# Optimization experiments

Measured on AMD Instinct MI355X. Metric: run time of the kernel, lower is better.

## Reference

```python
import jax, jax.numpy as jnp
import numpy as np

B, S, D = 8, 2048, 768

def setup_inputs():
    key = jax.random.key(0)
    k1, k2, k3, k4 = jax.random.split(key, 4)
    hidden = jax.random.normal(k1, (B, S, D), dtype=jnp.float32)
    # relative lengths in [0.5, 1.0) so every sequence has a realistic valid region
    lengths = 0.5 + 0.5 * jax.random.uniform(k2, (B,), dtype=jnp.float32)
    s = 1.0 / np.sqrt(D)
    W1 = jax.random.uniform(k3, (D, D), minval=-s, maxval=s, dtype=jnp.float32)
    b1 = jnp.zeros((D,), jnp.float32)
    W2 = jax.random.uniform(k4, (D,), minval=-s, maxval=s, dtype=jnp.float32)
    b2 = jnp.zeros((), jnp.float32)
    return {"hidden": hidden, "lengths": lengths, "W1": W1, "b1": b1, "W2": W2, "b2": b2}

def _boundaries(hidden, lengths, W1, b1, W2, b2):
    # Eval-mode boundary prediction (dropout = identity, soft = probs).
    Bn, Sn, _ = hidden.shape
    actual_lens = (lengths * Sn).astype(jnp.int32)                      # [B]
    valid = (jnp.arange(Sn)[None, :] < actual_lens[:, None]).astype(hidden.dtype)  # [B,S]
    h = jax.nn.gelu(hidden @ W1 + b1, approximate=False)                # torch nn.GELU is exact
    logits = h @ W2 + b2                                                # [B,S]
    probs = jax.nn.sigmoid(logits)
    soft = probs * valid
    hard = (probs > 0.5).astype(hidden.dtype) * valid
    last_valid = jnp.clip(actual_lens - 1, 0, Sn - 1)
    bi = jnp.arange(Bn)
    soft = soft.at[bi, last_valid].set(1.0)
    hard = hard.at[bi, last_valid].set(1.0)
    hard_b = hard - jax.lax.stop_gradient(soft) + soft                  # straight-through
    return hard_b, probs * valid, valid, actual_lens

def reference(hidden, lengths, W1, b1, W2, b2):
    Bn, Sn, Dn = hidden.shape
    hard_b, masked_probs, valid, actual_lens = _boundaries(hidden, lengths, W1, b1, W2, b2)
    # K = max segments in the batch (data-dependent -> computed eagerly, as
    # the original torch code does with .item() inside common()).
    K = int(jnp.max(jnp.sum(jax.lax.stop_gradient(hard_b), axis=1)))
    # segment id of each position: boundary token ENDS its segment
    seg_id = jnp.cumsum(hard_b, axis=1) - hard_b                        # [B,S]
    seg_onehot = (jnp.arange(K)[None, None, :]
                  == jax.lax.stop_gradient(seg_id)[:, :, None])          # [B,S,K] == (foo==0)
    segment_mask = seg_onehot.astype(hidden.dtype) * valid[:, :, None]
    counts = jnp.maximum(segment_mask.sum(axis=1), 1.0)                 # [B,K]
    # dense one-hot mask-matmul segment mean, matching the torch bmm formulation
    pooled = jnp.einsum('bsk,bsd->bkd', segment_mask, hidden) / counts[:, :, None]
    nb = (hard_b * valid).sum(axis=1)                                   # boundaries / sample
    max_segments = max(K, 1)
    full = nb >= max_segments - 1
    partial = (nb > 0) & (nb < max_segments - 1)
    shortened = jnp.where(full, 1.0,
                          jnp.where(partial, (nb + 1.0) / max_segments, 0.0))
    return pooled, masked_probs, shortened, nb, actual_lens.astype(jnp.float32)
```

## Files before the change

### kernel.cpp

```cpp
#include <hip/hip_runtime.h>
#include <math.h>

typedef __bf16 bf16x8 __attribute__((ext_vector_type(8)));
typedef float  f32x4  __attribute__((ext_vector_type(4)));

#define NT2 12

__device__ inline float gelu_f(float x) {
    return 0.5f * x * (1.0f + erff(x * 0.70710678118654752f));
}

typedef const __attribute__((address_space(1))) void* gas_t;
typedef __attribute__((address_space(3))) void*       las_t;
__device__ __forceinline__ void gl_lds16(const void* g, void* l) {
    __builtin_amdgcn_global_load_lds((gas_t)g, (las_t)l, 16, 0, 0);
}

__global__ __launch_bounds__(256) void s0_w1t(
    const float* __restrict__ W1, __bf16* __restrict__ Wt, int Dn)
{
    __shared__ float tile[32][33];
    const int k0 = blockIdx.x * 32;
    const int n0 = blockIdx.y * 32;
    const int tx = threadIdx.x & 31, ty = threadIdx.x >> 5;
    #pragma unroll
    for (int p = 0; p < 4; ++p)
        tile[ty + p * 8][tx] = W1[(size_t)(k0 + ty + p * 8) * Dn + n0 + tx];
    __syncthreads();
    #pragma unroll
    for (int p = 0; p < 4; ++p) {
        const int n = n0 + ty + p * 8, k = k0 + tx;
        Wt[(size_t)n * Dn + k] = (__bf16)tile[tx][ty + p * 8];
    }
}

__global__ __launch_bounds__(512) void k1_f32(
    const float* __restrict__ X, const __bf16* __restrict__ W1t,
    const float* __restrict__ b1, const float* __restrict__ W2,
    float* __restrict__ partial, int Kd)
{
    __shared__ float  Asf[2][128 * 32];
    __shared__ __bf16 Bsh[2][128 * 32];

    const int t    = threadIdx.x;
    const int lane = t & 63;
    const int w    = t >> 6;
    const int wr   = w >> 1;
    const int wc   = w & 1;
    const int ln15 = lane & 15, lg = lane >> 4;
    const int m0   = blockIdx.x * 128;
    const int n0   = blockIdx.y * 128;

    const int ar0 = t >> 3, alc = t & 7;
    const int ar1 = ar0 + 64;
    const float* gA0 = X + (size_t)(m0 + ar0) * Kd + (alc ^ (ar0 & 7)) * 4;
    const float* gA1 = X + (size_t)(m0 + ar1) * Kd + (alc ^ (ar1 & 7)) * 4;

    const int brow = t >> 2;
    const int bkw  = (t & 3) ^ ((brow >> 1) & 3);
    const __bf16* gB = W1t + (size_t)(n0 + brow) * Kd + bkw * 8;

    int aoff0[2], aoff1[2], boff[4];
    #pragma unroll
    for (int mf = 0; mf < 2; ++mf) {
        const int r = wr * 32 + mf * 16 + ln15;
        aoff0[mf] = r * 32 + ((2 * lg)     ^ (r & 7)) * 4;
        aoff1[mf] = r * 32 + ((2 * lg + 1) ^ (r & 7)) * 4;
    }
    #pragma unroll
    for (int nf = 0; nf < 4; ++nf) {
        const int r = wc * 64 + nf * 16 + ln15;
        boff[nf] = r * 32 + (lg ^ ((r >> 1) & 3)) * 8;
    }

    f32x4 acc[2][4];
    #pragma unroll
    for (int i = 0; i < 2; ++i)
        #pragma unroll
        for (int j = 0; j < 4; ++j)
            acc[i][j] = (f32x4){0.f, 0.f, 0.f, 0.f};

    gl_lds16(gA0, &Asf[0][t * 4]);
    gl_lds16(gA1, &Asf[0][(t + 512) * 4]);
    gl_lds16(gB,  &Bsh[0][t * 8]);
    __syncthreads();

    const int nt = Kd / 32;
    int cur = 0;
    for (int kt = 0; kt < nt; ++kt) {
        if (kt + 1 < nt) {
            const int ko = (kt + 1) * 32;
            gl_lds16(gA0 + ko, &Asf[cur ^ 1][t * 4]);
            gl_lds16(gA1 + ko, &Asf[cur ^ 1][(t + 512) * 4]);
            gl_lds16(gB  + ko, &Bsh[cur ^ 1][t * 8]);
        }
        bf16x8 fa[2], fb[4];
        #pragma unroll
        for (int mf = 0; mf < 2; ++mf) {
            const f32x4 lo = *(const f32x4*)&Asf[cur][aoff0[mf]];
            const f32x4 hi = *(const f32x4*)&Asf[cur][aoff1[mf]];
            #pragma unroll
            for (int i = 0; i < 4; ++i) {
                fa[mf][i]     = (__bf16)lo[i];
                fa[mf][4 + i] = (__bf16)hi[i];
            }
        }
        #pragma unroll
        for (int nf = 0; nf < 4; ++nf)
            fb[nf] = *(const bf16x8*)&Bsh[cur][boff[nf]];
        #pragma unroll
        for (int mf = 0; mf < 2; ++mf)
            #pragma unroll
            for (int nf = 0; nf < 4; ++nf)
                acc[mf][nf] = __builtin_amdgcn_mfma_f32_16x16x32_bf16(
                    fa[mf], fb[nf], acc[mf][nf], 0, 0, 0);
        __syncthreads();
        cur ^= 1;
    }

    float b1v[4], w2v[4];
    #pragma unroll
    for (int nf = 0; nf < 4; ++nf) {
        const int n = n0 + wc * 64 + nf * 16 + ln15;
        b1v[nf] = b1[n];
        w2v[nf] = W2[n];
    }
    #pragma unroll
    for (int mf = 0; mf < 2; ++mf)
        #pragma unroll
        for (int j = 0; j < 4; ++j) {
            float s = 0.f;
            #pragma unroll
            for (int nf = 0; nf < 4; ++nf) {
                float c = acc[mf][nf][j] + b1v[nf];
                s += gelu_f(c) * w2v[nf];
            }
            s += __shfl_xor(s, 1);
            s += __shfl_xor(s, 2);
            s += __shfl_xor(s, 4);
            s += __shfl_xor(s, 8);
            if (ln15 == 0) {
                const int m = m0 + wr * 32 + mf * 16 + lg * 4 + j;
                partial[(size_t)m * NT2 + blockIdx.y * 2 + wc] = s;
            }
        }
}

__global__ __launch_bounds__(256) void k2a_logits(
    const float* __restrict__ partial, const float* __restrict__ lengths,
    const float* __restrict__ b2p, float* __restrict__ logits,
    float* __restrict__ out_probs, int S)
{
    const int idx = blockIdx.x * 256 + threadIdx.x;
    const int b = idx / S, s = idx - b * S;
    float sum = b2p[0];
    #pragma unroll
    for (int jt = 0; jt < NT2; ++jt)
        sum += partial[(size_t)idx * NT2 + jt];
    logits[idx] = sum;
    const int len = (int)(lengths[b] * (float)S);
    out_probs[idx] = (s < len) ? 1.0f / (1.0f + expf(-sum)) : 0.0f;
}

__global__ __launch_bounds__(256) void k2b_scan(
    const float* __restrict__ logits, const float* __restrict__ lengths,
    float* __restrict__ out_short, float* __restrict__ out_nb,
    float* __restrict__ out_lens, int* __restrict__ bpos,
    int* __restrict__ nb_arr, int S, int K)
{
    const int b = blockIdx.x;
    const int t = threadIdx.x;
    const int len = (int)(lengths[b] * (float)S);

    __shared__ int cnt[256];
    __shared__ int flags_s[2048];

    const int RP = S / 256;
    const int base_s = t * RP;
    int local = 0;
    #pragma unroll
    for (int r = 0; r < 8; ++r) {
        int s = base_s + r;
        bool v = (s < len);
        int f = (s == len - 1) ? 1 : ((v && logits[(size_t)b * S + s] > 0.0f) ? 1 : 0);
        flags_s[s] = f;
        local += f;
    }
    cnt[t] = local;
    __syncthreads();
    for (int off = 1; off < 256; off <<= 1) {
        int v = cnt[t];
        int u = (t >= off) ? cnt[t - off] : 0;
        __syncthreads();
        cnt[t] = v + u;
        __syncthreads();
    }
    int excl = cnt[t] - local;
    int total = cnt[255];
    for (int r = 0; r < RP; ++r) {
        int s = base_s + r;
        if (flags_s[s]) { bpos[b * S + excl] = s; ++excl; }
    }
    if (t == 0) {
        nb_arr[b] = total;
        float nbf = (float)total;
        float Kf  = (float)K;
        out_nb[b]   = nbf;
        out_lens[b] = (float)len;
        float sh;
        if (nbf >= Kf - 1.0f)      sh = 1.0f;
        else if (nbf > 0.0f)       sh = (nbf + 1.0f) / Kf;
        else                       sh = 0.0f;
        out_short[b] = sh;
    }
}

__global__ __launch_bounds__(192) void k3_pool(
    const float* __restrict__ X, const int* __restrict__ bpos,
    const int* __restrict__ nb_arr, float* __restrict__ pooled,
    int S, int D, int K)
{
    const int bk = blockIdx.x;
    const int b  = bk / K;
    const int k  = bk - b * K;
    const int t  = threadIdx.x;
    const int nb = nb_arr[b];

    float4 acc = {0.f, 0.f, 0.f, 0.f};
    if (k < nb) {
        int start = (k == 0) ? 0 : (bpos[b * S + k - 1] + 1);
        int end   = bpos[b * S + k] + 1;
        float cntf = (float)(end - start);
        for (int s = start; s < end; ++s) {
            const float4 v = *(const float4*)&X[((size_t)b * S + s) * D + t * 4];
            acc.x += v.x; acc.y += v.y; acc.z += v.z; acc.w += v.w;
        }
        acc.x /= cntf; acc.y /= cntf; acc.z /= cntf; acc.w /= cntf;
    }
    *(float4*)&pooled[((size_t)b * K + k) * D + t * 4] = acc;
}

extern "C" void kernel_launch(void* const* d_in, const int* in_sizes, int n_in,
                              void* d_out, int out_size, void* d_ws, size_t ws_size,
                              hipStream_t stream) {
    const float* hidden  = (const float*)d_in[0];
    const float* lengths = (const float*)d_in[1];
    const float* W1      = (const float*)d_in[2];
    const float* b1      = (const float*)d_in[3];
    const float* W2      = (const float*)d_in[4];
    const float* b2      = (const float*)d_in[5];

    const int B = in_sizes[1];
    const int D = in_sizes[3];
    const int S = in_sizes[0] / (B * D);
    const int M = B * S;
    const int K = (out_size - B * S - 3 * B) / (B * D);

    float* out_pooled = (float*)d_out;
    float* out_probs  = out_pooled + (size_t)B * K * D;
    float* out_short  = out_probs + (size_t)B * S;
    float* out_nb     = out_short + B;
    float* out_lens   = out_nb + B;

    char* wsp = (char*)d_ws;
    float* partial = (float*)wsp; wsp += (size_t)M * NT2 * sizeof(float);
    float* logits  = (float*)wsp; wsp += (size_t)M * sizeof(float);
    int*   bpos    = (int*)wsp;   wsp += (size_t)M * sizeof(int);
    int*   nb_arr  = (int*)wsp;

    __bf16* W1t = (__bf16*)out_pooled;

    dim3 gs(D / 32, D / 32);
    s0_w1t<<<gs, 256, 0, stream>>>(W1, W1t, D);

    dim3 g1(M / 128, D / 128);
    k1_f32<<<g1, 512, 0, stream>>>(hidden, W1t, b1, W2, partial, D);

    k2a_logits<<<M / 256, 256, 0, stream>>>(partial, lengths, b2, logits,
                                            out_probs, S);
    k2b_scan<<<B, 256, 0, stream>>>(logits, lengths, out_short, out_nb,
                                    out_lens, bpos, nb_arr, S, K);
    k3_pool<<<B * K, D / 4, 0, stream>>>(hidden, bpos, nb_arr, out_pooled, S, D, K);
}
```

Measured before the change: 59.29 us.

## Pre-convert hidden to bf16, triple-buffer GEMM loads, pool from bf16 copy

Adds a pass that converts hidden to a bf16 workspace copy. The GEMM now streams bf16 A tiles through a three-stage LDS ring with explicit vmcnt waits and one barrier per k-step, instead of loading fp32 tiles and converting them in the inner loop. The segment pooling also reads the bf16 copy, which halves its read traffic but lowers the precision of the pooled means compared with the fp32 reference. The extra conversion pass adds a full read of hidden plus a bf16 write.

```diff
diff --git a/kernel.cpp b/kernel.cpp
--- a/kernel.cpp
+++ b/kernel.cpp
@@ -34,13 +34,29 @@
     }
 }
 
-__global__ __launch_bounds__(512) void k1_f32(
-    const float* __restrict__ X, const __bf16* __restrict__ W1t,
+__global__ __launch_bounds__(256) void s0_xb(
+    const float* __restrict__ X, __bf16* __restrict__ Xb, int n8)
+{
+    const int i = blockIdx.x * 256 + threadIdx.x;
+    if (i < n8) {
+        const float4 v0 = *(const float4*)(X + (size_t)i * 8);
+        const float4 v1 = *(const float4*)(X + (size_t)i * 8 + 4);
+        bf16x8 o;
+        o[0] = (__bf16)v0.x; o[1] = (__bf16)v0.y;
+        o[2] = (__bf16)v0.z; o[3] = (__bf16)v0.w;
+        o[4] = (__bf16)v1.x; o[5] = (__bf16)v1.y;
+        o[6] = (__bf16)v1.z; o[7] = (__bf16)v1.w;
+        *(bf16x8*)(Xb + (size_t)i * 8) = o;
+    }
+}
+
+__global__ __launch_bounds__(512) void k1_p3(
+    const __bf16* __restrict__ Xb, const __bf16* __restrict__ W1t,
     const float* __restrict__ b1, const float* __restrict__ W2,
     float* __restrict__ partial, int Kd)
 {
-    __shared__ float  Asf[2][128 * 32];
-    __shared__ __bf16 Bsh[2][128 * 32];
+    __shared__ __bf16 Ash[3][128 * 32];
+    __shared__ __bf16 Bsh[3][128 * 32];
 
     const int t    = threadIdx.x;
     const int lane = t & 63;
@@ -51,21 +67,16 @@
     const int m0   = blockIdx.x * 128;
     const int n0   = blockIdx.y * 128;
 
-    const int ar0 = t >> 3, alc = t & 7;
-    const int ar1 = ar0 + 64;
-    const float* gA0 = X + (size_t)(m0 + ar0) * Kd + (alc ^ (ar0 & 7)) * 4;
-    const float* gA1 = X + (size_t)(m0 + ar1) * Kd + (alc ^ (ar1 & 7)) * 4;
-
-    const int brow = t >> 2;
-    const int bkw  = (t & 3) ^ ((brow >> 1) & 3);
-    const __bf16* gB = W1t + (size_t)(n0 + brow) * Kd + bkw * 8;
-
-    int aoff0[2], aoff1[2], boff[4];
+    const int srow = t >> 2;
+    const int sgkw = (t & 3) ^ ((srow >> 1) & 3);
+    const __bf16* gA = Xb  + (size_t)(m0 + srow) * Kd + sgkw * 8;
+    const __bf16* gB = W1t + (size_t)(n0 + srow) * Kd + sgkw * 8;
+
+    int aoff[2], boff[4];
     #pragma unroll
     for (int mf = 0; mf < 2; ++mf) {
         const int r = wr * 32 + mf * 16 + ln15;
-        aoff0[mf] = r * 32 + ((2 * lg)     ^ (r & 7)) * 4;
-        aoff1[mf] = r * 32 + ((2 * lg + 1) ^ (r & 7)) * 4;
+        aoff[mf] = r * 32 + (lg ^ ((r >> 1) & 3)) * 8;
     }
     #pragma unroll
     for (int nf = 0; nf < 4; ++nf) {
@@ -80,43 +91,39 @@
         for (int j = 0; j < 4; ++j)
             acc[i][j] = (f32x4){0.f, 0.f, 0.f, 0.f};
 
-    gl_lds16(gA0, &Asf[0][t * 4]);
-    gl_lds16(gA1, &Asf[0][(t + 512) * 4]);
-    gl_lds16(gB,  &Bsh[0][t * 8]);
-    __syncthreads();
+    gl_lds16(gA,      &Ash[0][t * 8]);
+    gl_lds16(gB,      &Bsh[0][t * 8]);
+    gl_lds16(gA + 32, &Ash[1][t * 8]);
+    gl_lds16(gB + 32, &Bsh[1][t * 8]);
 
     const int nt = Kd / 32;
-    int cur = 0;
     for (int kt = 0; kt < nt; ++kt) {
-        if (kt + 1 < nt) {
-            const int ko = (kt + 1) * 32;
-            gl_lds16(gA0 + ko, &Asf[cur ^ 1][t * 4]);
-            gl_lds16(gA1 + ko, &Asf[cur ^ 1][(t + 512) * 4]);
-            gl_lds16(gB  + ko, &Bsh[cur ^ 1][t * 8]);
-        }
+        asm volatile("s_waitcnt vmcnt(2)" ::: "memory");
+        __builtin_amdgcn_s_barrier();
+        __builtin_amdgcn_sched_barrier(0);
+
+        const int cb = kt % 3;
         bf16x8 fa[2], fb[4];
         #pragma unroll
-        for (int mf = 0; mf < 2; ++mf) {
-            const f32x4 lo = *(const f32x4*)&Asf[cur][aoff0[mf]];
-            const f32x4 hi = *(const f32x4*)&Asf[cur][aoff1[mf]];
-            #pragma unroll
-            for (int i = 0; i < 4; ++i) {
-                fa[mf][i]     = (__bf16)lo[i];
-                fa[mf][4 + i] = (__bf16)hi[i];
-            }
-        }
+        for (int mf = 0; mf < 2; ++mf)
+            fa[mf] = *(const bf16x8*)&Ash[cb][aoff[mf]];
         #pragma unroll
         for (int nf = 0; nf < 4; ++nf)
-            fb[nf] = *(const bf16x8*)&Bsh[cur][boff[nf]];
+            fb[nf] = *(const bf16x8*)&Bsh[cb][boff[nf]];
         #pragma unroll
         for (int mf = 0; mf < 2; ++mf)
             #pragma unroll
             for (int nf = 0; nf < 4; ++nf)
                 acc[mf][nf] = __builtin_amdgcn_mfma_f32_16x16x32_bf16(
                     fa[mf], fb[nf], acc[mf][nf], 0, 0, 0);
-        __syncthreads();
-        cur ^= 1;
-    }
+
+        const int kn = (kt + 2 < nt) ? (kt + 2) : (nt - 1);
+        const int ko = kn * 32;
+        const int nb = (kt + 2) % 3;
+        gl_lds16(gA + ko, &Ash[nb][t * 8]);
+        gl_lds16(gB + ko, &Bsh[nb][t * 8]);
+    }
+    asm volatile("s_waitcnt vmcnt(0)" ::: "memory");
 
     float b1v[4], w2v[4];
     #pragma unroll
@@ -215,8 +222,8 @@
     }
 }
 
-__global__ __launch_bounds__(192) void k3_pool(
-    const float* __restrict__ X, const int* __restrict__ bpos,
+__global__ __launch_bounds__(192) void k3_pool_bf(
+    const __bf16* __restrict__ Xb, const int* __restrict__ bpos,
     const int* __restrict__ nb_arr, float* __restrict__ pooled,
     int S, int D, int K)
 {
@@ -232,8 +239,11 @@
         int end   = bpos[b * S + k] + 1;
         float cntf = (float)(end - start);
         for (int s = start; s < end; ++s) {
-            const float4 v = *(const float4*)&X[((size_t)b * S + s) * D + t * 4];
-            acc.x += v.x; acc.y += v.y; acc.z += v.z; acc.w += v.w;
+            const ushort4 u = *(const ushort4*)&Xb[((size_t)b * S + s) * D + t * 4];
+            acc.x += __builtin_bit_cast(float, (unsigned)u.x << 16);
+            acc.y += __builtin_bit_cast(float, (unsigned)u.y << 16);
+            acc.z += __builtin_bit_cast(float, (unsigned)u.z << 16);
+            acc.w += __builtin_bit_cast(float, (unsigned)u.w << 16);
         }
         acc.x /= cntf; acc.y /= cntf; acc.z /= cntf; acc.w /= cntf;
     }
@@ -263,6 +273,7 @@
     float* out_lens   = out_nb + B;
 
     char* wsp = (char*)d_ws;
+    __bf16* Xb = (__bf16*)wsp;    wsp += (size_t)M * D * sizeof(__bf16);
     float* partial = (float*)wsp; wsp += (size_t)M * NT2 * sizeof(float);
     float* logits  = (float*)wsp; wsp += (size_t)M * sizeof(float);
     int*   bpos    = (int*)wsp;   wsp += (size_t)M * sizeof(int);
@@ -273,12 +284,15 @@
     dim3 gs(D / 32, D / 32);
     s0_w1t<<<gs, 256, 0, stream>>>(W1, W1t, D);
 
+    const int n8 = M * D / 8;
+    s0_xb<<<(n8 + 255) / 256, 256, 0, stream>>>(hidden, Xb, n8);
+
     dim3 g1(M / 128, D / 128);
-    k1_f32<<<g1, 512, 0, stream>>>(hidden, W1t, b1, W2, partial, D);
+    k1_p3<<<g1, 512, 0, stream>>>(Xb, W1t, b1, W2, partial, D);
 
     k2a_logits<<<M / 256, 256, 0, stream>>>(partial, lengths, b2, logits,
                                             out_probs, S);
     k2b_scan<<<B, 256, 0, stream>>>(logits, lengths, out_short, out_nb,
                                     out_lens, bpos, nb_arr, S, K);
-    k3_pool<<<B * K, D / 4, 0, stream>>>(hidden, bpos, nb_arr, out_pooled, S, D, K);
-}
+    k3_pool_bf<<<B * K, D / 4, 0, stream>>>(Xb, bpos, nb_arr, out_pooled, S, D, K);
+}
```

After: 69.06 us. 16.5% more time.
